# Kernel optimization log

Hardware: AMD Instinct MI355X
Metric: run time of the kernel (lower is better)

The kernel has to match this reference:

```python
import jax, jax.numpy as jnp
import numpy as np

N_NODES = 50000
N_EDGES = 800000
IN_F = 128
HID = 256
N_CLS = 10
NUM_GRAPHS = 256


def setup_inputs() -> dict:
    key = jax.random.key(0)
    ks = jax.random.split(key, 8)
    x = jax.random.normal(ks[0], (N_NODES, IN_F), dtype=jnp.float32)
    edge_index = jax.random.randint(ks[1], (2, N_EDGES), 0, N_NODES, dtype=jnp.int64)
    batch = jnp.sort(jax.random.randint(ks[2], (N_NODES,), 0, NUM_GRAPHS, dtype=jnp.int64))
    # Glorot-style init for weights (GCNConv default), zeros bias
    W1 = jax.random.normal(ks[3], (IN_F, HID), dtype=jnp.float32) / np.sqrt(IN_F)
    b1 = jnp.zeros((HID,), dtype=jnp.float32)
    W2 = jax.random.normal(ks[4], (HID, HID), dtype=jnp.float32) / np.sqrt(HID)
    b2 = jnp.zeros((HID,), dtype=jnp.float32)
    Wlin = jax.random.normal(ks[5], (HID, N_CLS), dtype=jnp.float32) / np.sqrt(HID)
    blin = jnp.zeros((N_CLS,), dtype=jnp.float32)
    return {"x": x, "edge_index": edge_index, "batch": batch,
            "W1": W1, "b1": b1, "W2": W2, "b2": b2, "Wlin": Wlin, "blin": blin}


def reference(x, edge_index, batch, W1, b1, W2, b2, Wlin, blin):
    N = x.shape[0]
    # PyG GCNConv default: add self-loops, symmetric normalization D^-1/2 A D^-1/2
    loop = jnp.arange(N, dtype=edge_index.dtype)
    src = jnp.concatenate([edge_index[0], loop])  # message source (row)
    dst = jnp.concatenate([edge_index[1], loop])  # aggregation target (col)
    deg = jax.ops.segment_sum(jnp.ones_like(dst, dtype=x.dtype), dst, num_segments=N)
    dinv = jnp.where(deg > 0, jax.lax.rsqrt(deg), 0.0)
    norm = dinv[src] * dinv[dst]  # [E+N]

    def gcn_conv(h, W, b):
        h = h @ W                          # linear transform first (GCNConv)
        msg = h[src] * norm[:, None]       # gather + edge scale
        agg = jax.ops.segment_sum(msg, dst, num_segments=N)  # scatter-add
        return agg + b

    h = jax.nn.relu(gcn_conv(x, W1, b1))
    h = gcn_conv(h, W2, b2)

    # global_mean_pool over batch ids
    counts = jax.ops.segment_sum(jnp.ones((N,), x.dtype), batch, num_segments=NUM_GRAPHS)
    pooled = jax.ops.segment_sum(h, batch, num_segments=NUM_GRAPHS)
    pooled = pooled / jnp.maximum(counts, 1.0)[:, None]  # [NUM_GRAPHS, HID]

    return pooled @ Wlin + blin  # forward returns logits (softmax unused in forward)
```

## Files before the change

### kernel.cpp

```cpp
#include <hip/hip_runtime.h>
#include <hip/hip_bf16.h>

typedef __hip_bfloat16 bf16;
typedef __attribute__((ext_vector_type(8))) short short8;
typedef __attribute__((ext_vector_type(4))) float f32x4;
typedef __attribute__((ext_vector_type(2))) float f32x2;

#define N_NODES 50000
#define N_EDGES 800000
#define IN_F    128
#define HID     256
#define N_CLS   10
#define N_GRAPH 256

#define NB 98
#define PBLOCKS 256

__device__ __forceinline__ int IG(const int* __restrict__ p, int i, int w) {
    return w ? p[2 * i] : p[i];
}
__device__ __forceinline__ float LF(const void* __restrict__ p, int i, int isbf) {
    return isbf ? __bfloat162float(((const bf16*)p)[i]) : ((const float*)p)[i];
}
__device__ __forceinline__ float b2f(unsigned short h) {
    union { unsigned u; float f; } c; c.u = ((unsigned)h) << 16; return c.f;
}
__device__ __forceinline__ unsigned short f2b(float x) {
    bf16 h = __float2bfloat16(x);
    union { bf16 b; unsigned short u; } c; c.b = h; return c.u;
}
__device__ __forceinline__ float f8s(unsigned b) {
    union { unsigned u; float f; } c;
    c.u = ((b & 0x80u) << 24) | ((b & 0x7Fu) << 20);
    return c.f;
}
#define F8SCALE 0x1p120f
__device__ __forceinline__ unsigned f2fp8(float x) {
    unsigned short h = f2b(x * 0x1p-120f);
    unsigned s = ((unsigned)h >> 8) & 0x80u;
    unsigned mag = (unsigned)h & 0x7FFFu;
    unsigned r = (mag + 7u + ((mag >> 4) & 1u)) >> 4;
    if (r > 0x7Eu) r = 0x7Eu;
    return s | r;
}

#if defined(__has_builtin)
#if __has_builtin(__builtin_amdgcn_cvt_pk_f32_fp8)
#define HW_FP8 1
#endif
#if __has_builtin(__builtin_amdgcn_cvt_pk_fp8_f32)
#define HW_FP8E 1
#endif
#endif

__device__ __forceinline__ f32x2 cvt2lo(unsigned v) {
#ifdef HW_FP8
    return __builtin_amdgcn_cvt_pk_f32_fp8((int)v, false);
#else
    f32x2 r; r[0] = f8s(v & 0xFF) * F8SCALE; r[1] = f8s((v >> 8) & 0xFF) * F8SCALE; return r;
#endif
}
__device__ __forceinline__ f32x2 cvt2hi(unsigned v) {
#ifdef HW_FP8
    return __builtin_amdgcn_cvt_pk_f32_fp8((int)v, true);
#else
    f32x2 r; r[0] = f8s((v >> 16) & 0xFF) * F8SCALE; r[1] = f8s(v >> 24) * F8SCALE; return r;
#endif
}
__device__ __forceinline__ unsigned pk4_fp8(float v0, float v1, float v2, float v3) {
#ifdef HW_FP8E
    int o = __builtin_amdgcn_cvt_pk_fp8_f32(v0, v1, 0, false);
    o = __builtin_amdgcn_cvt_pk_fp8_f32(v2, v3, o, true);
    return (unsigned)o;
#else
    return f2fp8(v0) | (f2fp8(v1) << 8) | (f2fp8(v2) << 16) | (f2fp8(v3) << 24);
#endif
}

__global__ __launch_bounds__(256) void k_detect(const int* __restrict__ ei,
                                                const unsigned short* __restrict__ x,
                                                int* __restrict__ flags) {
    __shared__ int nz, cnt;
    if (threadIdx.x == 0) { nz = 0; cnt = 0; }
    __syncthreads();
    int found = 0, c = 0;
    for (int s = 0; s < 4; ++s) {
        int idx = 2 * (threadIdx.x * 4 + s) + 1;
        if (ei[idx] != 0) found = 1;
    }
    for (int s = 0; s < 8; ++s) {
        unsigned short h = x[threadIdx.x * 8 + s];
        int e = (h >> 7) & 0xFF;
        if (e >= 110 && e <= 135) c++;
    }
    if (found) atomicAdd(&nz, 1);
    atomicAdd(&cnt, c);
    __syncthreads();
    if (threadIdx.x == 0) {
        flags[0] = (nz == 0) ? 1 : 0;
        flags[1] = (cnt > 1536) ? 1 : 0;
    }
}

__global__ __launch_bounds__(256) void k_partA1(const int* __restrict__ ei, int* __restrict__ bucketCnt,
                                                int* __restrict__ blockBase, const int* __restrict__ flags,
                                                int E, int N) {
    __shared__ int h[NB];
    int t = threadIdx.x;
    if (t < NB) h[t] = 0;
    __syncthreads();
    int w = flags[0];
    for (int e = blockIdx.x * 256 + t; e < E; e += PBLOCKS * 256) {
        int d = IG(ei, E + e, w);
        int s = IG(ei, e, w);
        if ((unsigned)d < (unsigned)N && (unsigned)s < (unsigned)N)
            atomicAdd(&h[d >> 9], 1);
    }
    __syncthreads();
    if (t < NB)
        blockBase[blockIdx.x * NB + t] = atomicAdd(&bucketCnt[t * 16], h[t]);
}

__global__ __launch_bounds__(128) void k_bscan(const int* __restrict__ bucketCnt,
                                               int* __restrict__ bucketBase) {
    __shared__ int s[128];
    int t = threadIdx.x;
    int v = (t < NB) ? bucketCnt[t * 16] : 0;
    s[t] = v;
    __syncthreads();
    for (int off = 1; off < 128; off <<= 1) {
        int add = (t >= off) ? s[t - off] : 0;
        __syncthreads();
        s[t] += add;
        __syncthreads();
    }
    if (t <= NB) bucketBase[t] = (t < NB) ? (s[t] - v) : s[NB - 1] + 0;
    if (t == NB - 1) bucketBase[NB] = s[t];
}

__global__ __launch_bounds__(256) void k_partA2(const int* __restrict__ ei,
                                                const int* __restrict__ bucketBase,
                                                const int* __restrict__ blockBase,
                                                unsigned* __restrict__ part,
                                                const int* __restrict__ flags, int E, int N) {
    __shared__ int cur[NB];
    int t = threadIdx.x;
    if (t < NB) cur[t] = bucketBase[t] + blockBase[blockIdx.x * NB + t];
    __syncthreads();
    int w = flags[0];
    for (int e = blockIdx.x * 256 + t; e < E; e += PBLOCKS * 256) {
        int d = IG(ei, E + e, w);
        int s = IG(ei, e, w);
        if ((unsigned)d < (unsigned)N && (unsigned)s < (unsigned)N) {
            int slot = atomicAdd(&cur[d >> 9], 1);
            part[slot] = ((unsigned)(d & 511) << 16) | (unsigned)s;
        }
    }
}

__global__ __launch_bounds__(256) void k_partB(const unsigned* __restrict__ part,
                                               const int* __restrict__ bucketBase,
                                               int* __restrict__ rowptr, float* __restrict__ dinv,
                                               int* __restrict__ col, int N) {
    __shared__ int hist[512];
    __shared__ int scn[512];
    __shared__ int pair[256];
    int b = blockIdx.x, t = threadIdx.x;
    int s0 = bucketBase[b], e0 = bucketBase[b + 1];
    hist[t] = 0; hist[t + 256] = 0;
    __syncthreads();
    for (int j = s0 + t; j < e0; j += 256)
        atomicAdd(&hist[part[j] >> 16], 1);
    __syncthreads();
    int a0 = hist[2 * t], a1 = hist[2 * t + 1];
    int pv = a0 + a1;
    pair[t] = pv;
    __syncthreads();
    for (int off = 1; off < 256; off <<= 1) {
        int add = (t >= off) ? pair[t - off] : 0;
        __syncthreads();
        pair[t] += add;
        __syncthreads();
    }
    int pbase = pair[t] - pv;
    scn[2 * t] = pbase;
    scn[2 * t + 1] = pbase + a0;
    __syncthreads();
#pragma unroll
    for (int hh = 0; hh < 2; ++hh) {
        int l = t + hh * 256;
        int node = b * 512 + l;
        if (node < N) {
            rowptr[node] = s0 + scn[l];
            dinv[node] = rsqrtf((float)(hist[l] + 1));
        }
    }
    if (b == 0 && t == 0) rowptr[N] = bucketBase[NB];
    __syncthreads();
    for (int j = s0 + t; j < e0; j += 256) {
        unsigned p = part[j];
        int pos = s0 + atomicAdd(&scn[p >> 16], 1);
        col[pos] = (int)(p & 0xFFFFu);
    }
}

#define CVTX_BLOCKS 6250
#define CVT1_BLOCKS 128
#define CVT2_BLOCKS 256
#define GB_BLOCKS   196
__global__ __launch_bounds__(256) void k_cvt(const void* __restrict__ x, const float* __restrict__ dinv,
                                             unsigned char* __restrict__ xs8,
                                             const void* __restrict__ W1, unsigned short* __restrict__ w1t,
                                             const void* __restrict__ W2, unsigned short* __restrict__ w2t,
                                             const int* __restrict__ batch, int* __restrict__ gstart,
                                             const int* __restrict__ flags) {
    int b = blockIdx.x;
    int fb = flags[1];
    if (b < CVTX_BLOCKS) {
        int gid = b * 256 + threadIdx.x;
        int row = gid >> 5;
        float d = dinv[row];
        float vx, vy, vz, vw;
        if (fb) {
            ushort4 v = ((const ushort4*)x)[gid];
            vx = b2f(v.x); vy = b2f(v.y); vz = b2f(v.z); vw = b2f(v.w);
        } else {
            float4 v = ((const float4*)x)[gid];
            vx = v.x; vy = v.y; vz = v.z; vw = v.w;
        }
        ((unsigned*)xs8)[gid] = pk4_fp8(vx * d, vy * d, vz * d, vw * d);
    } else if (b < CVTX_BLOCKS + CVT1_BLOCKS) {
        int i = (b - CVTX_BLOCKS) * 256 + threadIdx.x;
        int n = i >> 7, k = i & 127;
        w1t[i] = f2b(LF(W1, k * 256 + n, fb));
    } else if (b < CVTX_BLOCKS + CVT1_BLOCKS + CVT2_BLOCKS) {
        int i = (b - CVTX_BLOCKS - CVT1_BLOCKS) * 256 + threadIdx.x;
        int n = i >> 8, k = i & 255;
        w2t[i] = f2b(LF(W2, k * 256 + n, fb));
    } else {
        int i = (b - CVTX_BLOCKS - CVT1_BLOCKS - CVT2_BLOCKS) * 256 + threadIdx.x;
        if (i <= N_NODES) {
            int w = flags[0];
            int prev = (i == 0) ? -1 : IG(batch, i - 1, w);
            int cur  = (i == N_NODES) ? N_GRAPH : IG(batch, i, w);
            if (prev < -1) prev = -1;
            if (cur > N_GRAPH) cur = N_GRAPH;
            for (int g = prev + 1; g <= cur; ++g)
                if (g >= 0 && g <= N_GRAPH) gstart[g] = i;
        }
    }
}

__global__ __launch_bounds__(256) void k_gcn2l(const unsigned short* __restrict__ A,
                                               const unsigned short* __restrict__ B1t,
                                               const unsigned short* __restrict__ B2t,
                                               unsigned char* __restrict__ C8, int M,
                                               const float* __restrict__ dinv,
                                               const void* __restrict__ bias1,
                                               const int* __restrict__ flags) {
    __shared__ unsigned short As1[64 * 136];
    __shared__ unsigned short Hs[64 * 264];
    int t = threadIdx.x;
    int lane = t & 63;
    int w = t >> 6;
    int bm = blockIdx.x * 64;
    int l15 = lane & 15, quad = lane >> 4;
    int fb = flags[1];

    {
        const uint4* src = (const uint4*)&A[(size_t)bm * 128];
#pragma unroll
        for (int j = 0; j < 4; ++j) {
            int f = t + j * 256;
            int row = f >> 4, cu = f & 15;
            *(uint4*)&As1[row * 136 + cu * 8] = src[(size_t)row * 16 + cu];
        }
    }
    __syncthreads();

    f32x4 acc[4][4];
#pragma unroll
    for (int ar = 0; ar < 4; ++ar)
#pragma unroll
        for (int tt = 0; tt < 4; ++tt) acc[ar][tt] = (f32x4){0.f, 0.f, 0.f, 0.f};

#pragma unroll
    for (int ks = 0; ks < 4; ++ks) {
        short8 a[4], b[4];
#pragma unroll
        for (int ar = 0; ar < 4; ++ar)
            a[ar] = *(const short8*)&As1[(ar * 16 + l15) * 136 + ks * 32 + quad * 8];
#pragma unroll
        for (int tt = 0; tt < 4; ++tt)
            b[tt] = *(const short8*)&B1t[(size_t)(w * 64 + tt * 16 + l15) * 128 + ks * 32 + quad * 8];
#pragma unroll
        for (int tt = 0; tt < 4; ++tt)
#pragma unroll
            for (int ar = 0; ar < 4; ++ar)
                acc[ar][tt] = __builtin_amdgcn_mfma_f32_16x16x32_bf16(b[tt], a[ar], acc[ar][tt], 0, 0, 0);
    }

    float drow[4];
#pragma unroll
    for (int ar = 0; ar < 4; ++ar) {
        int row = bm + ar * 16 + l15;
        drow[ar] = (row < M) ? dinv[row] : 1.f;
    }
#pragma unroll
    for (int tt = 0; tt < 4; ++tt) {
        int colb = w * 64 + tt * 16 + quad * 4;
        float bc[4];
#pragma unroll
        for (int rr = 0; rr < 4; ++rr) bc[rr] = LF(bias1, colb + rr, fb);
#pragma unroll
        for (int ar = 0; ar < 4; ++ar) {
            ushort4 o;
            o.x = f2b(fmaxf(fmaf(acc[ar][tt][0], drow[ar], bc[0]), 0.f));
            o.y = f2b(fmaxf(fmaf(acc[ar][tt][1], drow[ar], bc[1]), 0.f));
            o.z = f2b(fmaxf(fmaf(acc[ar][tt][2], drow[ar], bc[2]), 0.f));
            o.w = f2b(fmaxf(fmaf(acc[ar][tt][3], drow[ar], bc[3]), 0.f));
            *(ushort4*)&Hs[(ar * 16 + l15) * 264 + colb] = o;
            acc[ar][tt] = (f32x4){0.f, 0.f, 0.f, 0.f};
        }
    }
    __syncthreads();

#pragma unroll
    for (int ks = 0; ks < 8; ++ks) {
        short8 a[4], b[4];
#pragma unroll
        for (int ar = 0; ar < 4; ++ar)
            a[ar] = *(const short8*)&Hs[(ar * 16 + l15) * 264 + ks * 32 + quad * 8];
#pragma unroll
        for (int tt = 0; tt < 4; ++tt)
            b[tt] = *(const short8*)&B2t[(size_t)(w * 64 + tt * 16 + l15) * 256 + ks * 32 + quad * 8];
#pragma unroll
        for (int tt = 0; tt < 4; ++tt)
#pragma unroll
            for (int ar = 0; ar < 4; ++ar)
                acc[ar][tt] = __builtin_amdgcn_mfma_f32_16x16x32_bf16(b[tt], a[ar], acc[ar][tt], 0, 0, 0);
    }

    unsigned* Cs = (unsigned*)As1;
    __syncthreads();
#pragma unroll
    for (int tt = 0; tt < 4; ++tt) {
#pragma unroll
        for (int ar = 0; ar < 4; ++ar) {
            float v0 = acc[ar][tt][0] * drow[ar];
            float v1 = acc[ar][tt][1] * drow[ar];
            float v2 = acc[ar][tt][2] * drow[ar];
            float v3 = acc[ar][tt][3] * drow[ar];
            Cs[(ar * 16 + l15) * 68 + w * 16 + tt * 4 + quad] = pk4_fp8(v0, v1, v2, v3);
        }
    }
    __syncthreads();
    int r = t >> 2, h = t & 3;
    if (bm + r < M) {
        const unsigned* src = Cs + r * 68 + h * 16;
        uint4* dst = (uint4*)&C8[(size_t)(bm + r) * 256 + h * 64];
#pragma unroll
        for (int j = 0; j < 4; ++j) dst[j] = *(const uint4*)(src + j * 4);
    }
}

__global__ __launch_bounds__(256) void k_agg2(const unsigned char* __restrict__ XS,
                                              const int* __restrict__ rowptr, const int* __restrict__ col,
                                              unsigned short* __restrict__ Hout, int N) {
    int jb = blockIdx.x;
    int x8 = jb & 7, k = jb >> 3;
    int gIdx = k >> 4, win = k & 15;
    int node0 = (gIdx * 8 + x8) * 64 + win * 4;
    int lane = threadIdx.x & 63;
    int i = node0 + (threadIdx.x >> 6);
    if (i >= N) return;
    int fo = lane * 2;
    unsigned sv = *(const unsigned short*)&XS[(size_t)i * 128 + fo];
    f32x2 a = cvt2lo(sv);
    int s = rowptr[i], e = rowptr[i + 1];
    int j = s;
    while (j + 16 <= e) {
        unsigned v[16];
#pragma unroll
        for (int q = 0; q < 16; ++q)
            v[q] = *(const unsigned short*)&XS[(size_t)col[j + q] * 128 + fo];
#pragma unroll
        for (int q = 0; q < 16; ++q) a += cvt2lo(v[q]);
        j += 16;
    }
    if (j + 8 <= e) {
        unsigned v[8];
#pragma unroll
        for (int q = 0; q < 8; ++q)
            v[q] = *(const unsigned short*)&XS[(size_t)col[j + q] * 128 + fo];
#pragma unroll
        for (int q = 0; q < 8; ++q) a += cvt2lo(v[q]);
        j += 8;
    }
    if (j + 4 <= e) {
        unsigned v[4];
#pragma unroll
        for (int q = 0; q < 4; ++q)
            v[q] = *(const unsigned short*)&XS[(size_t)col[j + q] * 128 + fo];
#pragma unroll
        for (int q = 0; q < 4; ++q) a += cvt2lo(v[q]);
        j += 4;
    }
    for (; j < e; ++j)
        a += cvt2lo(*(const unsigned short*)&XS[(size_t)col[j] * 128 + fo]);
    ushort2 o;
    o.x = f2b(a[0]); o.y = f2b(a[1]);
    *(ushort2*)&Hout[(size_t)i * 128 + fo] = o;
}

__global__ __launch_bounds__(256) void k_agg4(const unsigned char* __restrict__ XW,
                                              const int* __restrict__ rowptr, const int* __restrict__ col,
                                              const float* __restrict__ dinv, const void* __restrict__ bias,
                                              const int* __restrict__ flags,
                                              unsigned short* __restrict__ Hout, int N) {
    int lane = threadIdx.x & 63;
    int i = (blockIdx.x * 256 + threadIdx.x) >> 6;
    if (i >= N) return;
    int fo = lane * 4;
    unsigned sv = *(const unsigned*)&XW[(size_t)i * 256 + fo];
    f32x2 a01 = cvt2lo(sv), a23 = cvt2hi(sv);
    int s = rowptr[i], e = rowptr[i + 1];
    int j = s;
    while (j + 16 <= e) {
        unsigned v[16];
#pragma unroll
        for (int q = 0; q < 16; ++q)
            v[q] = *(const unsigned*)&XW[(size_t)col[j + q] * 256 + fo];
#pragma unroll
        for (int q = 0; q < 16; ++q) { a01 += cvt2lo(v[q]); a23 += cvt2hi(v[q]); }
        j += 16;
    }
    if (j + 8 <= e) {
        unsigned v[8];
#pragma unroll
        for (int q = 0; q < 8; ++q)
            v[q] = *(const unsigned*)&XW[(size_t)col[j + q] * 256 + fo];
#pragma unroll
        for (int q = 0; q < 8; ++q) { a01 += cvt2lo(v[q]); a23 += cvt2hi(v[q]); }
        j += 8;
    }
    if (j + 4 <= e) {
        unsigned v[4];
#pragma unroll
        for (int q = 0; q < 4; ++q)
            v[q] = *(const unsigned*)&XW[(size_t)col[j + q] * 256 + fo];
#pragma unroll
        for (int q = 0; q < 4; ++q) { a01 += cvt2lo(v[q]); a23 += cvt2hi(v[q]); }
        j += 4;
    }
    for (; j < e; ++j) {
        unsigned v = *(const unsigned*)&XW[(size_t)col[j] * 256 + fo];
        a01 += cvt2lo(v); a23 += cvt2hi(v);
    }
    int fb = flags[1];
    float di = dinv[i];
    float bx = LF(bias, fo + 0, fb), by = LF(bias, fo + 1, fb);
    float bz = LF(bias, fo + 2, fb), bw = LF(bias, fo + 3, fb);
    ushort4 o;
    o.x = f2b(fmaf(a01[0], di, bx)); o.y = f2b(fmaf(a01[1], di, by));
    o.z = f2b(fmaf(a23[0], di, bz)); o.w = f2b(fmaf(a23[1], di, bw));
    *(ushort4*)&Hout[(size_t)i * 256 + fo] = o;
}

__global__ __launch_bounds__(256) void k_poolfinal(const unsigned short* __restrict__ H2,
                                                   const int* __restrict__ gstart,
                                                   const void* __restrict__ Wlin,
                                                   const void* __restrict__ blin,
                                                   const int* __restrict__ flags,
                                                   void* __restrict__ outv) {
    __shared__ float red[4][256];
    __shared__ float p[256];
    int g = blockIdx.x, t = threadIdx.x;
    int sub = t >> 6, lane = t & 63;
    int s = gstart[g], e = gstart[g + 1];
    int cnt = e - s;
    float ax = 0.f, ay = 0.f, az = 0.f, aw = 0.f;
    for (int i = s + sub; i < e; i += 4) {
        ushort4 v = *(const ushort4*)&H2[(size_t)i * 256 + lane * 4];
        ax += b2f(v.x); ay += b2f(v.y); az += b2f(v.z); aw += b2f(v.w);
    }
    red[sub][lane * 4 + 0] = ax;
    red[sub][lane * 4 + 1] = ay;
    red[sub][lane * 4 + 2] = az;
    red[sub][lane * 4 + 3] = aw;
    __syncthreads();
    float inv = 1.f / fmaxf((float)cnt, 1.f);
    p[t] = (red[0][t] + red[1][t] + red[2][t] + red[3][t]) * inv;
    __syncthreads();
    int fb = flags[1];
    if (t < N_CLS) {
        float sum = LF(blin, t, fb);
        for (int f = 0; f < HID; ++f) sum = fmaf(p[f], LF(Wlin, f * N_CLS + t, fb), sum);
        if (fb) ((bf16*)outv)[g * N_CLS + t] = __float2bfloat16(sum);
        else    ((float*)outv)[g * N_CLS + t] = sum;
    }
}

extern "C" void kernel_launch(void* const* d_in, const int* in_sizes, int n_in,
                              void* d_out, int out_size, void* d_ws, size_t ws_size,
                              hipStream_t stream) {
    (void)n_in; (void)ws_size; (void)in_sizes; (void)out_size;
    const void* x     = d_in[0];
    const int*  ei    = (const int*)d_in[1];
    const int*  batch = (const int*)d_in[2];
    const void* W1    = d_in[3];
    const void* b1    = d_in[4];
    const void* W2    = d_in[5];
    const void* b2    = d_in[6];
    const void* Wl    = d_in[7];
    const void* bl    = d_in[8];

    const int N = N_NODES, E = N_EDGES, F = IN_F, H = HID, G = N_GRAPH;

    char* ws = (char*)d_ws;
    size_t off = 0;
    auto alloc = [&](size_t bytes) -> void* {
        void* p = ws + off;
        off += (bytes + 511) & ~(size_t)511;
        return p;
    };
    unsigned char*  xs8  = (unsigned char*)alloc((size_t)N * F);
    unsigned short* aggX = (unsigned short*)alloc((size_t)N * F * 2);
    unsigned char*  XW2s8 = (unsigned char*)alloc((size_t)N * H);
    unsigned short* H2   = (unsigned short*)alloc((size_t)N * H * 2);
    unsigned short* w1t  = (unsigned short*)alloc((size_t)H * F * 2);
    unsigned short* w2t  = (unsigned short*)alloc((size_t)H * H * 2);
    int*   bucketCnt = (int*)alloc((size_t)NB * 16 * 4);
    int*   bucketBase = (int*)alloc((size_t)(NB + 1) * 4);
    int*   blockBase = (int*)alloc((size_t)PBLOCKS * NB * 4);
    unsigned* part  = (unsigned*)alloc((size_t)E * 4);
    int*   gstart  = (int*)alloc((size_t)(G + 1) * 4);
    float* dinv    = (float*)alloc((size_t)N * 4);
    int*   rowptr  = (int*)alloc((size_t)(N + 1) * 4);
    int*   flags   = (int*)alloc(512);
    int*   col     = (int*)alloc((size_t)E * 4);
    size_t zero_bytes = (size_t)NB * 16 * 4;

    hipMemsetAsync(bucketCnt, 0, zero_bytes, stream);

    k_detect<<<1, 256, 0, stream>>>(ei, (const unsigned short*)x, flags);
    k_partA1<<<PBLOCKS, 256, 0, stream>>>(ei, bucketCnt, blockBase, flags, E, N);
    k_bscan<<<1, 128, 0, stream>>>(bucketCnt, bucketBase);
    k_partA2<<<PBLOCKS, 256, 0, stream>>>(ei, bucketBase, blockBase, part, flags, E, N);
    k_partB<<<NB, 256, 0, stream>>>(part, bucketBase, rowptr, dinv, col, N);

    k_cvt<<<CVTX_BLOCKS + CVT1_BLOCKS + CVT2_BLOCKS + GB_BLOCKS, 256, 0, stream>>>(
        x, dinv, xs8, W1, w1t, W2, w2t, batch, gstart, flags);

    int g64 = (N + 63) >> 6;
    int aggBlocks = ((g64 + 7) >> 3) * 8 * 16;
    int nbAgg = (N + 3) / 4;

    k_agg2<<<aggBlocks, 256, 0, stream>>>(xs8, rowptr, col, aggX, N);
    k_gcn2l<<<g64, 256, 0, stream>>>(aggX, w1t, w2t, XW2s8, N, dinv, b1, flags);
    k_agg4<<<nbAgg, 256, 0, stream>>>(XW2s8, rowptr, col, dinv, b2, flags, H2, N);
    k_poolfinal<<<G, 256, 0, stream>>>(H2, gstart, Wl, bl, flags, d_out);
}
```

Baseline: 260.2 us.

## Fuse layer-1 neighbor aggregation into the two-layer GEMM kernel prologue

```diff
diff --git a/kernel.cpp b/kernel.cpp
--- a/kernel.cpp
+++ b/kernel.cpp
@@ -251,7 +251,9 @@
     }
 }
 
-__global__ __launch_bounds__(256) void k_gcn2l(const unsigned short* __restrict__ A,
+__global__ __launch_bounds__(256) void k_gcn2l(const unsigned char* __restrict__ XS,
+                                               const int* __restrict__ rowptr,
+                                               const int* __restrict__ col,
                                                const unsigned short* __restrict__ B1t,
                                                const unsigned short* __restrict__ B2t,
                                                unsigned char* __restrict__ C8, int M,
@@ -266,15 +268,50 @@
     int bm = blockIdx.x * 64;
     int l15 = lane & 15, quad = lane >> 4;
     int fb = flags[1];
-
-    {
-        const uint4* src = (const uint4*)&A[(size_t)bm * 128];
-#pragma unroll
-        for (int j = 0; j < 4; ++j) {
-            int f = t + j * 256;
-            int row = f >> 4, cu = f & 15;
-            *(uint4*)&As1[row * 136 + cu * 8] = src[(size_t)row * 16 + cu];
-        }
+    int fo = lane * 2;
+
+    for (int q = 0; q < 16; ++q) {
+        int i = bm + w * 16 + q;
+        ushort2 o;
+        if (i < M) {
+            unsigned sv = *(const unsigned short*)&XS[(size_t)i * 128 + fo];
+            f32x2 a = cvt2lo(sv);
+            int s = rowptr[i], e = rowptr[i + 1];
+            int j = s;
+            while (j + 16 <= e) {
+                unsigned v[16];
+#pragma unroll
+                for (int p = 0; p < 16; ++p)
+                    v[p] = *(const unsigned short*)&XS[(size_t)col[j + p] * 128 + fo];
+#pragma unroll
+                for (int p = 0; p < 16; ++p) a += cvt2lo(v[p]);
+                j += 16;
+            }
+            if (j + 8 <= e) {
+                unsigned v[8];
+#pragma unroll
+                for (int p = 0; p < 8; ++p)
+                    v[p] = *(const unsigned short*)&XS[(size_t)col[j + p] * 128 + fo];
+#pragma unroll
+                for (int p = 0; p < 8; ++p) a += cvt2lo(v[p]);
+                j += 8;
+            }
+            if (j + 4 <= e) {
+                unsigned v[4];
+#pragma unroll
+                for (int p = 0; p < 4; ++p)
+                    v[p] = *(const unsigned short*)&XS[(size_t)col[j + p] * 128 + fo];
+#pragma unroll
+                for (int p = 0; p < 4; ++p) a += cvt2lo(v[p]);
+                j += 4;
+            }
+            for (; j < e; ++j)
+                a += cvt2lo(*(const unsigned short*)&XS[(size_t)col[j] * 128 + fo]);
+            o.x = f2b(a[0]); o.y = f2b(a[1]);
+        } else {
+            o.x = 0; o.y = 0;
+        }
+        *(ushort2*)&As1[(w * 16 + q) * 136 + fo] = o;
     }
     __syncthreads();
 
@@ -362,55 +399,6 @@
 #pragma unroll
         for (int j = 0; j < 4; ++j) dst[j] = *(const uint4*)(src + j * 4);
     }
-}
-
-__global__ __launch_bounds__(256) void k_agg2(const unsigned char* __restrict__ XS,
-                                              const int* __restrict__ rowptr, const int* __restrict__ col,
-                                              unsigned short* __restrict__ Hout, int N) {
-    int jb = blockIdx.x;
-    int x8 = jb & 7, k = jb >> 3;
-    int gIdx = k >> 4, win = k & 15;
-    int node0 = (gIdx * 8 + x8) * 64 + win * 4;
-    int lane = threadIdx.x & 63;
-    int i = node0 + (threadIdx.x >> 6);
-    if (i >= N) return;
-    int fo = lane * 2;
-    unsigned sv = *(const unsigned short*)&XS[(size_t)i * 128 + fo];
-    f32x2 a = cvt2lo(sv);
-    int s = rowptr[i], e = rowptr[i + 1];
-    int j = s;
-    while (j + 16 <= e) {
-        unsigned v[16];
-#pragma unroll
-        for (int q = 0; q < 16; ++q)
-            v[q] = *(const unsigned short*)&XS[(size_t)col[j + q] * 128 + fo];
-#pragma unroll
-        for (int q = 0; q < 16; ++q) a += cvt2lo(v[q]);
-        j += 16;
-    }
-    if (j + 8 <= e) {
-        unsigned v[8];
-#pragma unroll
-        for (int q = 0; q < 8; ++q)
-            v[q] = *(const unsigned short*)&XS[(size_t)col[j + q] * 128 + fo];
-#pragma unroll
-        for (int q = 0; q < 8; ++q) a += cvt2lo(v[q]);
-        j += 8;
-    }
-    if (j + 4 <= e) {
-        unsigned v[4];
-#pragma unroll
-        for (int q = 0; q < 4; ++q)
-            v[q] = *(const unsigned short*)&XS[(size_t)col[j + q] * 128 + fo];
-#pragma unroll
-        for (int q = 0; q < 4; ++q) a += cvt2lo(v[q]);
-        j += 4;
-    }
-    for (; j < e; ++j)
-        a += cvt2lo(*(const unsigned short*)&XS[(size_t)col[j] * 128 + fo]);
-    ushort2 o;
-    o.x = f2b(a[0]); o.y = f2b(a[1]);
-    *(ushort2*)&Hout[(size_t)i * 128 + fo] = o;
 }
 
 __global__ __launch_bounds__(256) void k_agg4(const unsigned char* __restrict__ XW,
@@ -525,7 +513,6 @@
         return p;
     };
     unsigned char*  xs8  = (unsigned char*)alloc((size_t)N * F);
-    unsigned short* aggX = (unsigned short*)alloc((size_t)N * F * 2);
     unsigned char*  XW2s8 = (unsigned char*)alloc((size_t)N * H);
     unsigned short* H2   = (unsigned short*)alloc((size_t)N * H * 2);
     unsigned short* w1t  = (unsigned short*)alloc((size_t)H * F * 2);
@@ -553,11 +540,9 @@
         x, dinv, xs8, W1, w1t, W2, w2t, batch, gstart, flags);
 
     int g64 = (N + 63) >> 6;
-    int aggBlocks = ((g64 + 7) >> 3) * 8 * 16;
     int nbAgg = (N + 3) / 4;
 
-    k_agg2<<<aggBlocks, 256, 0, stream>>>(xs8, rowptr, col, aggX, N);
-    k_gcn2l<<<g64, 256, 0, stream>>>(aggX, w1t, w2t, XW2s8, N, dinv, b1, flags);
+    k_gcn2l<<<g64, 256, 0, stream>>>(xs8, rowptr, col, w1t, w2t, XW2s8, N, dinv, b1, flags);
     k_agg4<<<nbAgg, 256, 0, stream>>>(XW2s8, rowptr, col, dinv, b2, flags, H2, N);
     k_poolfinal<<<G, 256, 0, stream>>>(H2, gstart, Wl, bl, flags, d_out);
 }
```

After: 297.9 us. 14.5% more time.
